# Kernel optimization log

Hardware: AMD Instinct MI355X
Metric: run time of the kernel (lower is better)

The kernel has to match this reference:

```python
import jax, jax.numpy as jnp
import numpy as np

N = 100000
E = 1600000
D = 128
L = 2
NEG_SLOPE = 0.2
LN_EPS = 1e-5


def setup_inputs() -> dict:
    key = jax.random.key(0)
    ks = jax.random.split(key, 12)
    x = jax.random.normal(ks[0], (N, D), dtype=jnp.float32)
    src = jax.random.randint(ks[1], (E,), 0, N)
    dst = jax.random.randint(ks[2], (E,), 0, N)
    dst = jnp.where(src == dst, (dst + 1) % N, dst)  # no pre-existing self-loops
    edge_index = jnp.stack([src, dst]).astype(jnp.int64)
    edge_weight = jax.random.uniform(ks[3], (E,), dtype=jnp.float32)
    s = 1.0 / np.sqrt(D)
    W = jax.random.normal(ks[4], (L, D, D), dtype=jnp.float32) * s
    att_src = jax.random.normal(ks[5], (L, D), dtype=jnp.float32) * s
    att_dst = jax.random.normal(ks[6], (L, D), dtype=jnp.float32) * s
    lin_edge_w = jax.random.normal(ks[7], (L, D), dtype=jnp.float32) * s  # Linear(1, D) weight
    att_edge = jax.random.normal(ks[8], (L, D), dtype=jnp.float32) * s
    bias = jnp.zeros((L, D), dtype=jnp.float32)
    ln_gamma = jnp.ones((D,), dtype=jnp.float32)
    ln_beta = jnp.zeros((D,), dtype=jnp.float32)
    return {"x": x, "edge_index": edge_index, "edge_weight": edge_weight,
            "W": W, "att_src": att_src, "att_dst": att_dst,
            "lin_edge_w": lin_edge_w, "att_edge": att_edge, "bias": bias,
            "ln_gamma": ln_gamma, "ln_beta": ln_beta}


def _gat_layer(x, src_f, dst_f, ew_f, W, a_src, a_dst, lew, a_edge, b):
    # x: [N, D]; src_f/dst_f/ew_f already include self-loops -> [E+N]
    h = x @ W                      # [N, D]
    alpha_s = h @ a_src            # [N]
    alpha_d = h @ a_dst            # [N]
    # edge_attr = ew[:,None] * lew; (edge_attr * att_edge).sum(-1) == ew * (lew . att_edge)
    alpha_e = ew_f * jnp.dot(lew, a_edge)           # [E+N]
    logits = jax.nn.leaky_relu(alpha_s[src_f] + alpha_d[dst_f] + alpha_e, NEG_SLOPE)
    # segment softmax over incoming edges of each destination node
    m = jax.ops.segment_max(logits, dst_f, num_segments=N)   # every node has a self-loop
    p = jnp.exp(logits - m[dst_f])
    z = jax.ops.segment_sum(p, dst_f, num_segments=N)
    coef = p / z[dst_f]                                      # [E+N]
    out = jax.ops.segment_sum(h[src_f] * coef[:, None], dst_f, num_segments=N)
    return out + b


def reference(x, edge_index, edge_weight, W, att_src, att_dst, lin_edge_w, att_edge, bias, ln_gamma, ln_beta):
    src, dst = edge_index[0], edge_index[1]
    # add_self_loops with fill_value='mean': loop weight = mean of incoming edge weights
    deg = jax.ops.segment_sum(jnp.ones_like(edge_weight), dst, num_segments=N)
    loop_w = jax.ops.segment_sum(edge_weight, dst, num_segments=N) / jnp.maximum(deg, 1.0)
    ar = jnp.arange(N)
    src_f = jnp.concatenate([src, ar])
    dst_f = jnp.concatenate([dst, ar])
    ew_f = jnp.concatenate([edge_weight, loop_w])
    xx = x
    for l in range(L):
        xx = _gat_layer(xx, src_f, dst_f, ew_f, W[l], att_src[l], att_dst[l],
                        lin_edge_w[l], att_edge[l], bias[l])
        xx = jax.nn.gelu(xx, approximate=False)
    xx = x + xx
    mu = jnp.mean(xx, axis=-1, keepdims=True)
    var = jnp.mean((xx - mu) ** 2, axis=-1, keepdims=True)
    return (xx - mu) * jax.lax.rsqrt(var + LN_EPS) * ln_gamma + ln_beta
```

## Files before the change

kernel.cpp:

```cpp
#include <hip/hip_runtime.h>
#include <hip/hip_bf16.h>
#include <math.h>

#define N_NODES 100000
#define N_EDGES 1600000
#define D 128
#define NEG 0.2f
#define LN_EPS 1e-5f

#define GEMM_BLOCKS ((N_NODES + 63) / 64)
#define PLACE_BLOCKS ((N_EDGES + 1023) / 1024)
#define AGG_BLOCKS (N_NODES / 16)

typedef __attribute__((ext_vector_type(8))) short bf16x8;
typedef __attribute__((ext_vector_type(4))) float f32x4;

__device__ __forceinline__ float lrelu(float v){ return fmaxf(v, NEG * v); }
__device__ __forceinline__ float gelu_exact(float v){ return 0.5f * v * (1.0f + erff(v * 0.7071067811865476f)); }
__device__ __forceinline__ float wave_sum(float v){
#pragma unroll
  for (int o = 32; o; o >>= 1) v += __shfl_xor(v, o, 64);
  return v;
}
__device__ __forceinline__ unsigned short f2bf(float f){
  __hip_bfloat16 h = __float2bfloat16(f);
  return *(unsigned short*)&h;
}
__device__ __forceinline__ float bf_lo(unsigned u){ return __uint_as_float(u << 16); }
__device__ __forceinline__ float bf_hi(unsigned u){ return __uint_as_float(u & 0xFFFF0000u); }

__global__ __launch_bounds__(256) void k_prep(const float* __restrict__ W,
                                              unsigned short* __restrict__ wfrag,
                                              const float* __restrict__ lew,
                                              const float* __restrict__ ae,
                                              float* __restrict__ c_e){
  if (threadIdx.x < 128){
    int l = threadIdx.x >> 6;
    int lane = threadIdx.x & 63;
    const float* a = lew + l * D;
    const float* b = ae + l * D;
    float v = a[lane] * b[lane] + a[64 + lane] * b[64 + lane];
    v = wave_sum(v);
    if (lane == 0) c_e[l] = v;
  }
#pragma unroll
  for (int it = 0; it < 16; it++){
    int slot = it * 256 + threadIdx.x;
    int lane = slot & 63;
    int kc   = (slot >> 6) & 3;
    int ct   = (slot >> 8) & 7;
    int l    = (slot >> 11) & 1;
    int quad = lane >> 4, n = (lane & 15) + ct * 16;
    const float* Wl = W + l * D * D;
    bf16x8 v;
#pragma unroll
    for (int j = 0; j < 8; j++){
      int k = kc * 32 + quad * 8 + j;
      v[j] = (short)f2bf(Wl[k * D + n]);
    }
    *(bf16x8*)(wfrag + (size_t)slot * 8) = v;
  }
}

template<bool ABF>
__device__ __forceinline__ void gemm_mfma(int gb,
                                          const void* __restrict__ xin_,
                                          const unsigned short* __restrict__ wfrag_l,
                                          const float* __restrict__ att_s,
                                          const float* __restrict__ att_d,
                                          unsigned short* __restrict__ hb,
                                          float* __restrict__ alpha_s,
                                          float* __restrict__ alpha_d){
  __shared__ __align__(16) unsigned short hstage[64 * 136];
  int tid = threadIdx.x;
  int wv = tid >> 6, lane = tid & 63;
  int quad = lane >> 4, c15 = lane & 15;
  int row0 = gb * 64 + wv * 16;

  int arow = min(row0 + c15, N_NODES - 1);
  bf16x8 a[4];
  if constexpr (ABF){
    const unsigned short* xr = (const unsigned short*)xin_ + (size_t)arow * D;
#pragma unroll
    for (int kc = 0; kc < 4; kc++)
      a[kc] = *(const bf16x8*)(xr + kc * 32 + quad * 8);
  } else {
    const float* xr = (const float*)xin_ + (size_t)arow * D;
#pragma unroll
    for (int kc = 0; kc < 4; kc++){
      float4 p = *(const float4*)(xr + kc * 32 + quad * 8);
      float4 q = *(const float4*)(xr + kc * 32 + quad * 8 + 4);
      bf16x8 t;
      t[0] = (short)f2bf(p.x); t[1] = (short)f2bf(p.y);
      t[2] = (short)f2bf(p.z); t[3] = (short)f2bf(p.w);
      t[4] = (short)f2bf(q.x); t[5] = (short)f2bf(q.y);
      t[6] = (short)f2bf(q.z); t[7] = (short)f2bf(q.w);
      a[kc] = t;
    }
  }

  f32x4 acc[8];
#pragma unroll
  for (int ct = 0; ct < 8; ct++) acc[ct] = (f32x4){0.f, 0.f, 0.f, 0.f};

#pragma unroll
  for (int ct = 0; ct < 8; ct++){
#pragma unroll
    for (int kc = 0; kc < 4; kc++){
      bf16x8 b = *(const bf16x8*)(wfrag_l + ((size_t)(ct * 4 + kc) * 64 + lane) * 8);
      acc[ct] = __builtin_amdgcn_mfma_f32_16x16x32_bf16(a[kc], b, acc[ct], 0, 0, 0);
    }
  }

  float attsv[8], attdv[8];
#pragma unroll
  for (int ct = 0; ct < 8; ct++){
    attsv[ct] = att_s[ct * 16 + c15];
    attdv[ct] = att_d[ct * 16 + c15];
  }
#pragma unroll
  for (int reg = 0; reg < 4; reg++){
    float ps = 0.f, pd = 0.f;
#pragma unroll
    for (int ct = 0; ct < 8; ct++){
      ps += acc[ct][reg] * attsv[ct];
      pd += acc[ct][reg] * attdv[ct];
    }
#pragma unroll
    for (int o = 8; o; o >>= 1){
      ps += __shfl_xor(ps, o, 64);
      pd += __shfl_xor(pd, o, 64);
    }
    int row = row0 + quad * 4 + reg;
    if (c15 == reg && row < N_NODES){ alpha_s[row] = ps; alpha_d[row] = pd; }
  }

#pragma unroll
  for (int ct = 0; ct < 8; ct++)
#pragma unroll
    for (int reg = 0; reg < 4; reg++)
      hstage[(wv * 16 + quad * 4 + reg) * 136 + ct * 16 + c15] = f2bf(acc[ct][reg]);
  __syncthreads();
#pragma unroll
  for (int i = 0; i < 4; i++){
    int flat = i * 256 + tid;
    int row = flat >> 4, c = flat & 15;
    int grow = gb * 64 + row;
    if (grow < N_NODES)
      *(uint4*)(hb + (size_t)grow * D + c * 8) = *(const uint4*)(hstage + row * 136 + c * 8);
  }
}

__global__ __launch_bounds__(256, 4) void k_gemm1_place(const float* __restrict__ xin,
                                                        const unsigned short* __restrict__ wfrag,
                                                        const float* __restrict__ att_s,
                                                        const float* __restrict__ att_d,
                                                        unsigned short* __restrict__ hb,
                                                        float* __restrict__ alpha_s,
                                                        float* __restrict__ alpha_d,
                                                        const int* __restrict__ ei,
                                                        const float* __restrict__ ew,
                                                        int* __restrict__ counter,
                                                        int2* __restrict__ csr, int cap){
  if (blockIdx.x >= PLACE_BLOCKS){
    gemm_mfma<false>(blockIdx.x - PLACE_BLOCKS, xin, wfrag, att_s, att_d, hb, alpha_s, alpha_d);
  } else {
    int pb = blockIdx.x;
    int e0 = pb * 1024 + threadIdx.x;
    int ss[4], dd[4], pp[4]; float wwv[4]; bool va[4];
#pragma unroll
    for (int i = 0; i < 4; i++){
      int e = e0 + i * 256;
      va[i] = e < N_EDGES;
      ss[i] = va[i] ? ei[e] : 0;
      dd[i] = va[i] ? ei[N_EDGES + e] : 0;
      wwv[i] = va[i] ? ew[e] : 0.f;
    }
#pragma unroll
    for (int i = 0; i < 4; i++) if (va[i]) pp[i] = atomicAdd(&counter[dd[i]], 1);
#pragma unroll
    for (int i = 0; i < 4; i++)
      if (va[i] && pp[i] < cap)
        csr[(size_t)dd[i] * cap + pp[i]] = make_int2(ss[i], __float_as_int(wwv[i]));
  }
}

__global__ __launch_bounds__(256, 4) void k_gemm_alpha(const unsigned short* __restrict__ xin,
                                                       const unsigned short* __restrict__ wfrag,
                                                       const float* __restrict__ att_s,
                                                       const float* __restrict__ att_d,
                                                       unsigned short* __restrict__ hb,
                                                       float* __restrict__ alpha_s,
                                                       float* __restrict__ alpha_d){
  gemm_mfma<true>(blockIdx.x, xin, wfrag, att_s, att_d, hb, alpha_s, alpha_d);
}

template<bool LN>
__device__ __forceinline__ void agg_core(const unsigned short* __restrict__ hb,
                                         const float* __restrict__ alpha_s,
                                         const float* __restrict__ alpha_d,
                                         const int* __restrict__ counter,
                                         const int2* __restrict__ csr, int cap,
                                         float c,
                                         const float* __restrict__ bias_l,
                                         const float* __restrict__ xres,
                                         const float* __restrict__ gamma,
                                         const float* __restrict__ beta,
                                         int n, int cg, int qbase,
                                         float o[8]){
  int deg = counter[n];
  int dg = min(deg, cap);
  size_t rs = (size_t)n * cap;
  float ad = alpha_d[n];
  float as_n = alpha_s[n];

  uint4 u_self = *((const uint4*)(hb + (size_t)n * D) + cg);
  float4 b_lo = *(const float4*)(bias_l + cg * 8);
  float4 b_hi = *(const float4*)(bias_l + cg * 8 + 4);
  float4 xr_lo, xr_hi, g_lo, g_hi, bt_lo, bt_hi;
  if constexpr (LN){
    const float* xr = xres + (size_t)n * D + cg * 8;
    xr_lo = *(const float4*)(xr);
    xr_hi = *(const float4*)(xr + 4);
    g_lo  = *(const float4*)(gamma + cg * 8);
    g_hi  = *(const float4*)(gamma + cg * 8 + 4);
    bt_lo = *(const float4*)(beta + cg * 8);
    bt_hi = *(const float4*)(beta + cg * 8 + 4);
  }

  float z = 0.f, wsum = 0.f;
  float acc[8];
#pragma unroll
  for (int k = 0; k < 8; k++) acc[k] = 0.f;

  for (int base = 0; base < dg; base += 16){
    int j = base + cg;
    float p = 0.f; int s = n;
    if (j < dg){
      int2 eg = csr[rs + j];
      s = eg.x;
      float w = __int_as_float(eg.y);
      wsum += w;
      p = __expf(lrelu(alpha_s[s] + ad + c * w));
    }
    z += p;
#pragma unroll
    for (int i = 0; i < 16; i++){
      float pi = __shfl(p, qbase + i, 64);
      int   si = __shfl(s, qbase + i, 64);
      uint4 u = *((const uint4*)(hb + (size_t)si * D) + cg);
      acc[0] += pi * bf_lo(u.x); acc[1] += pi * bf_hi(u.x);
      acc[2] += pi * bf_lo(u.y); acc[3] += pi * bf_hi(u.y);
      acc[4] += pi * bf_lo(u.z); acc[5] += pi * bf_hi(u.z);
      acc[6] += pi * bf_lo(u.w); acc[7] += pi * bf_hi(u.w);
    }
  }
#pragma unroll
  for (int ofs = 8; ofs; ofs >>= 1){
    z += __shfl_xor(z, ofs, 64);
    wsum += __shfl_xor(wsum, ofs, 64);
  }

  float lw = wsum / fmaxf((float)deg, 1.0f);
  float ps = __expf(lrelu(as_n + ad + c * lw));
  z += ps;
  acc[0] += ps * bf_lo(u_self.x); acc[1] += ps * bf_hi(u_self.x);
  acc[2] += ps * bf_lo(u_self.y); acc[3] += ps * bf_hi(u_self.y);
  acc[4] += ps * bf_lo(u_self.z); acc[5] += ps * bf_hi(u_self.z);
  acc[6] += ps * bf_lo(u_self.w); acc[7] += ps * bf_hi(u_self.w);

  float inv = 1.0f / z;
  float bv[8] = {b_lo.x, b_lo.y, b_lo.z, b_lo.w, b_hi.x, b_hi.y, b_hi.z, b_hi.w};
#pragma unroll
  for (int k = 0; k < 8; k++) o[k] = gelu_exact(acc[k] * inv + bv[k]);

  if constexpr (LN){
    float xrv[8] = {xr_lo.x, xr_lo.y, xr_lo.z, xr_lo.w, xr_hi.x, xr_hi.y, xr_hi.z, xr_hi.w};
    float s1 = 0.f;
#pragma unroll
    for (int k = 0; k < 8; k++){ o[k] += xrv[k]; s1 += o[k]; }
#pragma unroll
    for (int ofs = 8; ofs; ofs >>= 1) s1 += __shfl_xor(s1, ofs, 64);
    float mu = s1 * (1.0f / D);
    float s2 = 0.f;
#pragma unroll
    for (int k = 0; k < 8; k++){ o[k] -= mu; s2 += o[k] * o[k]; }
#pragma unroll
    for (int ofs = 8; ofs; ofs >>= 1) s2 += __shfl_xor(s2, ofs, 64);
    float rinv = rsqrtf(s2 * (1.0f / D) + LN_EPS);
    float gv[8] = {g_lo.x, g_lo.y, g_lo.z, g_lo.w, g_hi.x, g_hi.y, g_hi.z, g_hi.w};
    float btv[8] = {bt_lo.x, bt_lo.y, bt_lo.z, bt_lo.w, bt_hi.x, bt_hi.y, bt_hi.z, bt_hi.w};
#pragma unroll
    for (int k = 0; k < 8; k++) o[k] = o[k] * rinv * gv[k] + btv[k];
  }
}

__global__ __launch_bounds__(256) void k_agg1_fused(const unsigned short* __restrict__ hb,
                                                    const float* __restrict__ alpha_s,
                                                    const float* __restrict__ alpha_d,
                                                    const int* __restrict__ counter,
                                                    const int2* __restrict__ csr, int cap,
                                                    const float* __restrict__ c_e,
                                                    const float* __restrict__ bias,
                                                    const unsigned short* __restrict__ wfrag2,
                                                    const float* __restrict__ att_s2,
                                                    const float* __restrict__ att_d2,
                                                    unsigned short* __restrict__ hb2,
                                                    float* __restrict__ alpha2_s,
                                                    float* __restrict__ alpha2_d){
  __shared__ __align__(16) unsigned short astage[16 * 136];
  __shared__ float apart_s[16], apart_d[16];
  int tid = threadIdx.x;
  int lane = tid & 63;
  int cg = lane & 15;
  int qbase = lane & 48;
  int n = blockIdx.x * 16 + (tid >> 4);

  float o[8];
  agg_core<false>(hb, alpha_s, alpha_d, counter, csr, cap, c_e[0],
                  bias, nullptr, nullptr, nullptr, n, cg, qbase, o);

  unsigned short ob[8];
#pragma unroll
  for (int k = 0; k < 8; k++) ob[k] = f2bf(o[k]);
  *(uint4*)(astage + (tid >> 4) * 136 + cg * 8) = *(const uint4*)ob;
  if (tid < 16){ apart_s[tid] = 0.f; apart_d[tid] = 0.f; }
  __syncthreads();

  int wv = tid >> 6;
  int quad = lane >> 4, c15 = lane & 15;
  bf16x8 a[4];
#pragma unroll
  for (int kc = 0; kc < 4; kc++)
    a[kc] = *(const bf16x8*)(astage + c15 * 136 + kc * 32 + quad * 8);

  f32x4 acc2[2];
  float attsv[2], attdv[2];
#pragma unroll
  for (int t = 0; t < 2; t++){
    int ct = wv * 2 + t;
    acc2[t] = (f32x4){0.f, 0.f, 0.f, 0.f};
#pragma unroll
    for (int kc = 0; kc < 4; kc++){
      bf16x8 b = *(const bf16x8*)(wfrag2 + ((size_t)(ct * 4 + kc) * 64 + lane) * 8);
      acc2[t] = __builtin_amdgcn_mfma_f32_16x16x32_bf16(a[kc], b, acc2[t], 0, 0, 0);
    }
    attsv[t] = att_s2[ct * 16 + c15];
    attdv[t] = att_d2[ct * 16 + c15];
  }

#pragma unroll
  for (int reg = 0; reg < 4; reg++){
    float ps = acc2[0][reg] * attsv[0] + acc2[1][reg] * attsv[1];
    float pd = acc2[0][reg] * attdv[0] + acc2[1][reg] * attdv[1];
#pragma unroll
    for (int ofs = 8; ofs; ofs >>= 1){
      ps += __shfl_xor(ps, ofs, 64);
      pd += __shfl_xor(pd, ofs, 64);
    }
    if (c15 == reg){
      atomicAdd(&apart_s[quad * 4 + reg], ps);
      atomicAdd(&apart_d[quad * 4 + reg], pd);
    }
  }
  __syncthreads();

#pragma unroll
  for (int t = 0; t < 2; t++){
    int ct = wv * 2 + t;
#pragma unroll
    for (int reg = 0; reg < 4; reg++)
      astage[(quad * 4 + reg) * 136 + ct * 16 + c15] = f2bf(acc2[t][reg]);
  }
  __syncthreads();

  {
    int row = tid >> 4, ccol = tid & 15;
    int grow = blockIdx.x * 16 + row;
    *(uint4*)(hb2 + (size_t)grow * D + ccol * 8) = *(const uint4*)(astage + row * 136 + ccol * 8);
  }
  if (tid < 16){
    int grow = blockIdx.x * 16 + tid;
    alpha2_s[grow] = apart_s[tid];
    alpha2_d[grow] = apart_d[tid];
  }
}

__global__ __launch_bounds__(256) void k_agg1_plain(const unsigned short* __restrict__ hb,
                                                    const float* __restrict__ alpha_s,
                                                    const float* __restrict__ alpha_d,
                                                    const int* __restrict__ counter,
                                                    const int2* __restrict__ csr, int cap,
                                                    const float* __restrict__ c_e,
                                                    const float* __restrict__ bias,
                                                    unsigned short* __restrict__ outp_bf){
  int tid = threadIdx.x;
  int lane = tid & 63;
  int cg = lane & 15;
  int qbase = lane & 48;
  int n = blockIdx.x * 16 + (tid >> 4);
  float o[8];
  agg_core<false>(hb, alpha_s, alpha_d, counter, csr, cap, c_e[0],
                  bias, nullptr, nullptr, nullptr, n, cg, qbase, o);
  unsigned short ob[8];
#pragma unroll
  for (int k = 0; k < 8; k++) ob[k] = f2bf(o[k]);
  *(uint4*)(outp_bf + (size_t)n * D + cg * 8) = *(const uint4*)ob;
}

__global__ __launch_bounds__(256) void k_agg2(const unsigned short* __restrict__ hb,
                                              const float* __restrict__ alpha_s,
                                              const float* __restrict__ alpha_d,
                                              const int* __restrict__ counter,
                                              const int2* __restrict__ csr, int cap,
                                              const float* __restrict__ c_e,
                                              const float* __restrict__ bias,
                                              const float* __restrict__ xres,
                                              const float* __restrict__ gamma,
                                              const float* __restrict__ beta,
                                              float* __restrict__ outp){
  int tid = threadIdx.x;
  int lane = tid & 63;
  int cg = lane & 15;
  int qbase = lane & 48;
  int n = blockIdx.x * 16 + (tid >> 4);
  float o[8];
  agg_core<true>(hb, alpha_s, alpha_d, counter, csr, cap, c_e[1],
                 bias + D, xres, gamma, beta, n, cg, qbase, o);
  float* orow = outp + (size_t)n * D + cg * 8;
  *(float4*)(orow)     = make_float4(o[0], o[1], o[2], o[3]);
  *(float4*)(orow + 4) = make_float4(o[4], o[5], o[6], o[7]);
}

extern "C" void kernel_launch(void* const* d_in, const int* in_sizes, int n_in,
                              void* d_out, int out_size, void* d_ws, size_t ws_size,
                              hipStream_t stream) {
  const float* x     = (const float*)d_in[0];
  const int*   ei    = (const int*)d_in[1];
  const float* ew    = (const float*)d_in[2];
  const float* W     = (const float*)d_in[3];
  const float* att_s = (const float*)d_in[4];
  const float* att_d = (const float*)d_in[5];
  const float* lew   = (const float*)d_in[6];
  const float* ae    = (const float*)d_in[7];
  const float* bias  = (const float*)d_in[8];
  const float* gamma = (const float*)d_in[9];
  const float* beta  = (const float*)d_in[10];
  float* out = (float*)d_out;

  const int N = N_NODES;

  size_t fixed = (size_t)(5 * N + 16) * 4 + 65536;
  size_t hbB = (size_t)N * D * 2;
  bool fused; int cap;
  if      (ws_size >= fixed + (size_t)N * 64 * 8 + 2 * hbB){ fused = true;  cap = 64; }
  else if (ws_size >= fixed + (size_t)N * 48 * 8 + 2 * hbB){ fused = true;  cap = 48; }
  else if (ws_size >= fixed + (size_t)N * 64 * 8 + hbB)    { fused = false; cap = 64; }
  else                                                     { fused = false; cap = 48; }

  int*   counter  = (int*)d_ws;
  float* alpha_s  = (float*)(counter + N);
  float* alpha_d  = alpha_s + N;
  float* alpha2_s = alpha_d + N;
  float* alpha2_d = alpha2_s + N;
  float* c_e      = alpha2_d + N;
  unsigned short* wfrag = (unsigned short*)(c_e + 16);
  int2*  csr      = (int2*)(wfrag + 32768);
  unsigned short* hb  = (unsigned short*)(csr + (size_t)N * cap);
  unsigned short* hb2 = hb + (size_t)N * D;

  hipMemsetAsync(counter, 0, (size_t)N * sizeof(int), stream);
  k_prep<<<1, 256, 0, stream>>>(W, wfrag, lew, ae, c_e);

  k_gemm1_place<<<GEMM_BLOCKS + PLACE_BLOCKS, 256, 0, stream>>>(
      x, wfrag, att_s, att_d, hb, alpha_s, alpha_d, ei, ew, counter, csr, cap);

  if (fused){
    k_agg1_fused<<<AGG_BLOCKS, 256, 0, stream>>>(
        hb, alpha_s, alpha_d, counter, csr, cap, c_e, bias,
        wfrag + 16384, att_s + D, att_d + D, hb2, alpha2_s, alpha2_d);
    k_agg2<<<AGG_BLOCKS, 256, 0, stream>>>(
        hb2, alpha2_s, alpha2_d, counter, csr, cap, c_e, bias, x, gamma, beta, out);
  } else {
    unsigned short* h1b = (unsigned short*)d_out;
    k_agg1_plain<<<AGG_BLOCKS, 256, 0, stream>>>(
        hb, alpha_s, alpha_d, counter, csr, cap, c_e, bias, h1b);
    k_gemm_alpha<<<GEMM_BLOCKS, 256, 0, stream>>>(
        h1b, wfrag + 16384, att_s + D, att_d + D, hb, alpha_s, alpha_d);
    k_agg2<<<AGG_BLOCKS, 256, 0, stream>>>(
        hb, alpha_s, alpha_d, counter, csr, cap, c_e, bias, x, gamma, beta, out);
  }
}
```

Baseline: 443.1 us.

## Pad per-node atomic counters to cache-line stride and peel first 32 edges

Gives each destination-node degree counter its own 64-byte slot (stride 16 ints) when the workspace is large enough. The aim is to cut contention among neighbouring counters' atomics during CSR placement, at the cost of a larger memset and strided counter reads. It also peels the first two 16-edge chunks of the aggregation loop so the edge loads and exp for both chunks are issued together before the gathers. The peeled block always runs its full 32 gathers, using the self index with zero weight for lanes past the degree, which adds wasted gathers for low-degree nodes.

After: 429.1 us. 3.2% less time.

```diff
diff --git a/kernel.cpp b/kernel.cpp
--- a/kernel.cpp
+++ b/kernel.cpp
@@ -160,7 +160,7 @@
                                                         float* __restrict__ alpha_d,
                                                         const int* __restrict__ ei,
                                                         const float* __restrict__ ew,
-                                                        int* __restrict__ counter,
+                                                        int* __restrict__ counter, int cstride,
                                                         int2* __restrict__ csr, int cap){
   if (blockIdx.x >= PLACE_BLOCKS){
     gemm_mfma<false>(blockIdx.x - PLACE_BLOCKS, xin, wfrag, att_s, att_d, hb, alpha_s, alpha_d);
@@ -177,7 +177,7 @@
       wwv[i] = va[i] ? ew[e] : 0.f;
     }
 #pragma unroll
-    for (int i = 0; i < 4; i++) if (va[i]) pp[i] = atomicAdd(&counter[dd[i]], 1);
+    for (int i = 0; i < 4; i++) if (va[i]) pp[i] = atomicAdd(&counter[dd[i] * cstride], 1);
 #pragma unroll
     for (int i = 0; i < 4; i++)
       if (va[i] && pp[i] < cap)
@@ -199,7 +199,7 @@
 __device__ __forceinline__ void agg_core(const unsigned short* __restrict__ hb,
                                          const float* __restrict__ alpha_s,
                                          const float* __restrict__ alpha_d,
-                                         const int* __restrict__ counter,
+                                         const int* __restrict__ counter, int cstride,
                                          const int2* __restrict__ csr, int cap,
                                          float c,
                                          const float* __restrict__ bias_l,
@@ -208,7 +208,7 @@
                                          const float* __restrict__ beta,
                                          int n, int cg, int qbase,
                                          float o[8]){
-  int deg = counter[n];
+  int deg = counter[n * cstride];
   int dg = min(deg, cap);
   size_t rs = (size_t)n * cap;
   float ad = alpha_d[n];
@@ -233,7 +233,45 @@
 #pragma unroll
   for (int k = 0; k < 8; k++) acc[k] = 0.f;
 
-  for (int base = 0; base < dg; base += 16){
+  {
+    float p = 0.f, p2 = 0.f; int s = n, s2 = n;
+    if (cg < dg){
+      int2 eg = csr[rs + cg];
+      s = eg.x;
+      float w = __int_as_float(eg.y);
+      wsum += w;
+      p = __expf(lrelu(alpha_s[s] + ad + c * w));
+    }
+    if (16 + cg < dg){
+      int2 eg = csr[rs + 16 + cg];
+      s2 = eg.x;
+      float w = __int_as_float(eg.y);
+      wsum += w;
+      p2 = __expf(lrelu(alpha_s[s2] + ad + c * w));
+    }
+    z += p + p2;
+#pragma unroll
+    for (int i = 0; i < 16; i++){
+      float pi = __shfl(p, qbase + i, 64);
+      int   si = __shfl(s, qbase + i, 64);
+      uint4 u = *((const uint4*)(hb + (size_t)si * D) + cg);
+      acc[0] += pi * bf_lo(u.x); acc[1] += pi * bf_hi(u.x);
+      acc[2] += pi * bf_lo(u.y); acc[3] += pi * bf_hi(u.y);
+      acc[4] += pi * bf_lo(u.z); acc[5] += pi * bf_hi(u.z);
+      acc[6] += pi * bf_lo(u.w); acc[7] += pi * bf_hi(u.w);
+    }
+#pragma unroll
+    for (int i = 0; i < 16; i++){
+      float pi = __shfl(p2, qbase + i, 64);
+      int   si = __shfl(s2, qbase + i, 64);
+      uint4 u = *((const uint4*)(hb + (size_t)si * D) + cg);
+      acc[0] += pi * bf_lo(u.x); acc[1] += pi * bf_hi(u.x);
+      acc[2] += pi * bf_lo(u.y); acc[3] += pi * bf_hi(u.y);
+      acc[4] += pi * bf_lo(u.z); acc[5] += pi * bf_hi(u.z);
+      acc[6] += pi * bf_lo(u.w); acc[7] += pi * bf_hi(u.w);
+    }
+  }
+  for (int base = 32; base < dg; base += 16){
     int j = base + cg;
     float p = 0.f; int s = n;
     if (j < dg){
@@ -298,7 +336,7 @@
 __global__ __launch_bounds__(256) void k_agg1_fused(const unsigned short* __restrict__ hb,
                                                     const float* __restrict__ alpha_s,
                                                     const float* __restrict__ alpha_d,
-                                                    const int* __restrict__ counter,
+                                                    const int* __restrict__ counter, int cstride,
                                                     const int2* __restrict__ csr, int cap,
                                                     const float* __restrict__ c_e,
                                                     const float* __restrict__ bias,
@@ -317,7 +355,7 @@
   int n = blockIdx.x * 16 + (tid >> 4);
 
   float o[8];
-  agg_core<false>(hb, alpha_s, alpha_d, counter, csr, cap, c_e[0],
+  agg_core<false>(hb, alpha_s, alpha_d, counter, cstride, csr, cap, c_e[0],
                   bias, nullptr, nullptr, nullptr, n, cg, qbase, o);
 
   unsigned short ob[8];
@@ -389,7 +427,7 @@
 __global__ __launch_bounds__(256) void k_agg1_plain(const unsigned short* __restrict__ hb,
                                                     const float* __restrict__ alpha_s,
                                                     const float* __restrict__ alpha_d,
-                                                    const int* __restrict__ counter,
+                                                    const int* __restrict__ counter, int cstride,
                                                     const int2* __restrict__ csr, int cap,
                                                     const float* __restrict__ c_e,
                                                     const float* __restrict__ bias,
@@ -400,7 +438,7 @@
   int qbase = lane & 48;
   int n = blockIdx.x * 16 + (tid >> 4);
   float o[8];
-  agg_core<false>(hb, alpha_s, alpha_d, counter, csr, cap, c_e[0],
+  agg_core<false>(hb, alpha_s, alpha_d, counter, cstride, csr, cap, c_e[0],
                   bias, nullptr, nullptr, nullptr, n, cg, qbase, o);
   unsigned short ob[8];
 #pragma unroll
@@ -411,7 +449,7 @@
 __global__ __launch_bounds__(256) void k_agg2(const unsigned short* __restrict__ hb,
                                               const float* __restrict__ alpha_s,
                                               const float* __restrict__ alpha_d,
-                                              const int* __restrict__ counter,
+                                              const int* __restrict__ counter, int cstride,
                                               const int2* __restrict__ csr, int cap,
                                               const float* __restrict__ c_e,
                                               const float* __restrict__ bias,
@@ -425,7 +463,7 @@
   int qbase = lane & 48;
   int n = blockIdx.x * 16 + (tid >> 4);
   float o[8];
-  agg_core<true>(hb, alpha_s, alpha_d, counter, csr, cap, c_e[1],
+  agg_core<true>(hb, alpha_s, alpha_d, counter, cstride, csr, cap, c_e[1],
                  bias + D, xres, gamma, beta, n, cg, qbase, o);
   float* orow = outp + (size_t)n * D + cg * 8;
   *(float4*)(orow)     = make_float4(o[0], o[1], o[2], o[3]);
@@ -450,16 +488,18 @@
 
   const int N = N_NODES;
 
-  size_t fixed = (size_t)(5 * N + 16) * 4 + 65536;
   size_t hbB = (size_t)N * D * 2;
-  bool fused; int cap;
-  if      (ws_size >= fixed + (size_t)N * 64 * 8 + 2 * hbB){ fused = true;  cap = 64; }
-  else if (ws_size >= fixed + (size_t)N * 48 * 8 + 2 * hbB){ fused = true;  cap = 48; }
-  else if (ws_size >= fixed + (size_t)N * 64 * 8 + hbB)    { fused = false; cap = 64; }
-  else                                                     { fused = false; cap = 48; }
+  size_t fixP = ((size_t)(16 * N) + 4 * N + 16) * 4 + 65536;
+  size_t fix1 = ((size_t)N + 4 * N + 16) * 4 + 65536;
+  int cstride; bool fused; int cap;
+  if      (ws_size >= fixP + (size_t)N * 64 * 8 + 2 * hbB){ cstride = 16; fused = true;  cap = 64; }
+  else if (ws_size >= fixP + (size_t)N * 48 * 8 + 2 * hbB){ cstride = 16; fused = true;  cap = 48; }
+  else if (ws_size >= fix1 + (size_t)N * 64 * 8 + 2 * hbB){ cstride = 1;  fused = true;  cap = 64; }
+  else if (ws_size >= fix1 + (size_t)N * 64 * 8 + hbB)    { cstride = 1;  fused = false; cap = 64; }
+  else                                                     { cstride = 1;  fused = false; cap = 48; }
 
   int*   counter  = (int*)d_ws;
-  float* alpha_s  = (float*)(counter + N);
+  float* alpha_s  = (float*)(counter + (size_t)N * cstride);
   float* alpha_d  = alpha_s + N;
   float* alpha2_s = alpha_d + N;
   float* alpha2_d = alpha2_s + N;
@@ -469,25 +509,25 @@
   unsigned short* hb  = (unsigned short*)(csr + (size_t)N * cap);
   unsigned short* hb2 = hb + (size_t)N * D;
 
-  hipMemsetAsync(counter, 0, (size_t)N * sizeof(int), stream);
+  hipMemsetAsync(counter, 0, (size_t)N * cstride * sizeof(int), stream);
   k_prep<<<1, 256, 0, stream>>>(W, wfrag, lew, ae, c_e);
 
   k_gemm1_place<<<GEMM_BLOCKS + PLACE_BLOCKS, 256, 0, stream>>>(
-      x, wfrag, att_s, att_d, hb, alpha_s, alpha_d, ei, ew, counter, csr, cap);
+      x, wfrag, att_s, att_d, hb, alpha_s, alpha_d, ei, ew, counter, cstride, csr, cap);
 
   if (fused){
     k_agg1_fused<<<AGG_BLOCKS, 256, 0, stream>>>(
-        hb, alpha_s, alpha_d, counter, csr, cap, c_e, bias,
+        hb, alpha_s, alpha_d, counter, cstride, csr, cap, c_e, bias,
         wfrag + 16384, att_s + D, att_d + D, hb2, alpha2_s, alpha2_d);
     k_agg2<<<AGG_BLOCKS, 256, 0, stream>>>(
-        hb2, alpha2_s, alpha2_d, counter, csr, cap, c_e, bias, x, gamma, beta, out);
+        hb2, alpha2_s, alpha2_d, counter, cstride, csr, cap, c_e, bias, x, gamma, beta, out);
   } else {
     unsigned short* h1b = (unsigned short*)d_out;
     k_agg1_plain<<<AGG_BLOCKS, 256, 0, stream>>>(
-        hb, alpha_s, alpha_d, counter, csr, cap, c_e, bias, h1b);
+        hb, alpha_s, alpha_d, counter, cstride, csr, cap, c_e, bias, h1b);
     k_gemm_alpha<<<GEMM_BLOCKS, 256, 0, stream>>>(
         h1b, wfrag + 16384, att_s + D, att_d + D, hb, alpha_s, alpha_d);
     k_agg2<<<AGG_BLOCKS, 256, 0, stream>>>(
-        hb, alpha_s, alpha_d, counter, csr, cap, c_e, bias, x, gamma, beta, out);
-  }
-}
+        hb, alpha_s, alpha_d, counter, cstride, csr, cap, c_e, bias, x, gamma, beta, out);
+  }
+}
```
